# Kernel optimization log

Hardware: AMD Instinct MI355X
Metric: run time of the kernel (lower is better)

## Reference

```python
import jax, jax.numpy as jnp
import numpy as np

BN_EPS = 1e-3  # keras BatchNormalization default epsilon

def _prelu(x, a):
    return jnp.maximum(x, 0) + a * jnp.minimum(x, 0)

def _bn(x, g, b, m, v):
    # inference-mode batchnorm with moving statistics
    return (x - m) * jax.lax.rsqrt(v + BN_EPS) * g + b

def setup_inputs() -> dict:
    key = jax.random.key(0)
    ks = jax.random.split(key, 24)
    B, D, V, L = 4096, 768, 200000, 200000
    F = 3 * D  # 2304 = qid|pos|neg concat
    n = lambda i, shape, s=0.05: jax.random.normal(ks[i], shape, jnp.float32) * s
    return dict(
        qid_embeddings=jax.random.normal(ks[0], (B, D), jnp.float32),
        node_embeddings=n(1, (V, D), 0.1),
        leaf_embeddings=n(2, (L, D), 0.1),
        positives=jax.random.randint(ks[3], (B,), 0, V),
        negetives=jax.random.randint(ks[4], (B,), 0, V),
        p_isleafs=jax.random.randint(ks[5], (B,), 0, 2),
        n_isleafs=jax.random.randint(ks[6], (B,), 0, 2),
        W00=n(7, (F, 36)), b00=jnp.zeros((36,)), a00=jnp.full((36,), 0.25),
        W01=n(8, (36, 1)), b01=jnp.zeros((1,)),
        W1=n(9, (F, 128)), b1=jnp.zeros((128,)), a1=jnp.full((128,), 0.25),
        g1=jnp.ones((128,)), be1=n(10, (128,), 0.1), m1=n(11, (128,), 0.1),
        v1=jax.random.uniform(ks[12], (128,)) + 0.5,
        W2=n(13, (128, 64)), b2=jnp.zeros((64,)), a2=jnp.full((64,), 0.25),
        g2=jnp.ones((64,)), be2=n(14, (64,), 0.1), m2=n(15, (64,), 0.1),
        v2=jax.random.uniform(ks[16], (64,)) + 0.5,
        W3=n(17, (64, 24)), b3=jnp.zeros((24,)), a3=jnp.full((24,), 0.25),
        g3=jnp.ones((24,)), be3=n(18, (24,), 0.1), m3=n(19, (24,), 0.1),
        v3=jax.random.uniform(ks[20], (24,)) + 0.5,
        W4=n(21, (24, 2)), b4=jnp.zeros((2,)),
    )

def reference(qid_embeddings, node_embeddings, leaf_embeddings, positives, negetives,
              p_isleafs, n_isleafs, W00, b00, a00, W01, b01,
              W1, b1, a1, g1, be1, m1, v1,
              W2, b2, a2, g2, be2, m2, v2,
              W3, b3, a3, g3, be3, m3, v3, W4, b4):
    # per-sample conditional embedding gather (leaf table vs internal node table)
    pos = jnp.where((p_isleafs == 1)[:, None], leaf_embeddings[positives], node_embeddings[positives])  # [B,D]
    neg = jnp.where((n_isleafs == 1)[:, None], leaf_embeddings[negetives], node_embeddings[negetives])  # [B,D]
    q = qid_embeddings  # [B,D]
    # attention block: small Dense(36)->Dense(1) scalar weight per sample
    feat = jnp.concatenate([q, pos, neg], axis=1)  # [B,3D]
    h = _prelu(feat @ W00 + b00, a00)              # [B,36]
    w = h @ W01 + b01                              # [B,1]
    item = jnp.concatenate([w * pos, w * neg, q], axis=1)  # [B,3D]
    # MLP 2304 -> 128 -> 64 -> 24 -> 2 (layer10/20/30 unused in original call)
    x = _bn(_prelu(item @ W1 + b1, a1), g1, be1, m1, v1)
    x = _bn(_prelu(x @ W2 + b2, a2), g2, be2, m2, v2)
    x = _bn(_prelu(x @ W3 + b3, a3), g3, be3, m3, v3)
    return jax.nn.softmax(x @ W4 + b4, axis=-1)  # [B,2]
```

## Files before the change

kernel.cpp:

```cpp
#include <hip/hip_runtime.h>
#include <hip/hip_bf16.h>

typedef _Float16 half8 __attribute__((ext_vector_type(8)));
typedef _Float16 half4v __attribute__((ext_vector_type(4)));
typedef float f32x4 __attribute__((ext_vector_type(4)));

#define NCOLS 176
#define TILE_ELEMS (NCOLS*32)
#define TILE_U16 (TILE_ELEMS/8)
#define WTSTR 40
#define XSTR2 2312
#define BM 16

#define OFF_A36 0
#define OFF_TQ  2560
#define OFF_TPN 10752
#define OFF_WV  18944
#define OFF_X1  19008
#define OFF_W2  27456
#define OFF_X2  43840
#define OFF_W3  48192
#define OFF_X3  51264
#define OFF_SCR 53056
#define SM_BYTES 77632

struct Params {
  const float *qid, *node, *leaf;
  const int *pos_idx, *neg_idx, *p_leaf, *n_leaf;
  const float *b00, *a00, *W01, *b01;
  const float *b1, *a1, *g1, *be1, *m1, *v1;
  const float *W2, *b2, *a2, *g2, *be2, *m2, *v2;
  const float *W3, *b3, *a3, *g3, *be3, *m3, *v3;
  const float *W4, *b4;
  const _Float16 *Wp;
  float *out;
};

__global__ __launch_bounds__(256) void pack_weights(const float* __restrict__ W00,
                                                    const float* __restrict__ W1,
                                                    _Float16* __restrict__ Wp) {
  int g = blockIdx.x;
  int s = g / 24, t = g - s * 24;
  int k0 = t * 32;
  int w1row0 = (s == 0) ? 1536 : (s == 1 ? 0 : 768);
  __shared__ _Float16 T[NCOLS][WTSTR];
  int tid = threadIdx.x;
  for (int u = tid; u < 1024; u += 256) {
    int kk = u >> 5, c4 = u & 31;
    float4 f = *(const float4*)(W1 + (size_t)(w1row0 + k0 + kk) * 128 + c4 * 4);
    int c = 48 + c4 * 4;
    T[c + 0][kk] = (_Float16)f.x; T[c + 1][kk] = (_Float16)f.y;
    T[c + 2][kk] = (_Float16)f.z; T[c + 3][kk] = (_Float16)f.w;
  }
  for (int u = tid; u < 1152; u += 256) {
    int kk = u / 36, c = u - kk * 36;
    T[c][kk] = (_Float16)W00[(size_t)(s * 768 + k0 + kk) * 36 + c];
  }
  for (int u = tid; u < 384; u += 256) {
    int kk = u & 31, c = 36 + (u >> 5);
    T[c][kk] = (_Float16)0.f;
  }
  __syncthreads();
  uint4* dst = (uint4*)(Wp + (size_t)g * TILE_ELEMS);
  for (int u = tid; u < TILE_U16; u += 256) {
    int c = u >> 2, q = u & 3;
    dst[u] = *(const uint4*)&T[c][q * 8];
  }
}

__global__ __launch_bounds__(512) void fused_main(Params p) {
  __shared__ __align__(16) char sm[SM_BYTES];
  __shared__ const float* Xbase[3][BM];

  _Float16* X   = (_Float16*)sm;
  float*    A36 = (float*)(sm + OFF_A36);
  float*    Tq  = (float*)(sm + OFF_TQ);
  float*    Tpn = (float*)(sm + OFF_TPN);
  float*    wv  = (float*)(sm + OFF_WV);
  float*    x1  = (float*)(sm + OFF_X1);
  _Float16* W2h = (_Float16*)(sm + OFF_W2);
  float*    x2  = (float*)(sm + OFF_X2);
  _Float16* W3h = (_Float16*)(sm + OFF_W3);
  float*    x3  = (float*)(sm + OFF_X3);
  float*    scr = (float*)(sm + OFF_SCR);

  const int tid  = threadIdx.x;
  const int wid  = tid >> 6;
  const int lane = tid & 63;
  const int lm   = lane & 15;
  const int hk   = lane >> 4;
  const int nw   = wid & 3;
  const int kg   = wid >> 2;
  const int m0   = blockIdx.x * BM;
  const bool HAS2 = (nw < 3);

  const uint4* Wp4 = (const uint4*)p.Wp;
  const int woff = ((nw * 48 + lm) << 2) + hk;

  uint4 P[4][3];
  auto ldWp = [&](int j) {
    int s = j / 12;
    int g = s * 24 + kg + 2 * (j - s * 12);
    const uint4* b = Wp4 + (size_t)g * TILE_U16 + woff;
    P[j & 3][0] = b[0]; P[j & 3][1] = b[64];
    if (HAS2) P[j & 3][2] = b[128];
  };

  ldWp(0); ldWp(1); ldWp(2); ldWp(3);

  if (tid < 3 * BM) {
    int s = tid >> 4, i = tid & 15;
    const float* base;
    if (s == 0) base = p.qid + (size_t)(m0 + i) * 768;
    else if (s == 1) {
      int idx = p.pos_idx[m0 + i];
      base = ((p.p_leaf[m0 + i] == 1) ? p.leaf : p.node) + (size_t)idx * 768;
    } else {
      int idx = p.neg_idx[m0 + i];
      base = ((p.n_leaf[m0 + i] == 1) ? p.leaf : p.node) + (size_t)idx * 768;
    }
    Xbase[s][i] = base;
  }

  float4 sregA[6], sregB[6];
  auto stageLoad = [&](int s, float4* sr) {
#pragma unroll
    for (int jj = 0; jj < 6; ++jj) {
      int v = tid + jj * 512;
      int i = v / 192, c4 = v - i * 192;
      const float* b = (s == 0) ? (p.qid + (size_t)(m0 + i) * 768) : Xbase[s][i];
      sr[jj] = ((const float4*)b)[c4];
    }
  };
  auto stageWrite = [&](int s, const float4* sr) {
#pragma unroll
    for (int jj = 0; jj < 6; ++jj) {
      int v = tid + jj * 512;
      int i = v / 192, c4 = v - i * 192;
      float4 f = sr[jj];
      half4v h = { (_Float16)f.x, (_Float16)f.y, (_Float16)f.z, (_Float16)f.w };
      *(half4v*)(X + i * XSTR2 + s * 768 + c4 * 4) = h;
    }
  };

  stageLoad(0, sregA);
  __syncthreads();
  stageLoad(1, sregB);
  stageWrite(0, sregA);
  __syncthreads();

  f32x4 accA[3] = {{0.f,0.f,0.f,0.f},{0.f,0.f,0.f,0.f},{0.f,0.f,0.f,0.f}};
  f32x4 accB[3] = {{0.f,0.f,0.f,0.f},{0.f,0.f,0.f,0.f},{0.f,0.f,0.f,0.f}};
  half8 av[3];

  auto ldA = [&](int g) -> half8 {
    return *(const half8*)(X + lm * XSTR2 + g * 32 + hk * 8);
  };
  auto comp = [&](int g, int slot, half8 a) {
    half8 b0 = __builtin_bit_cast(half8, P[slot][0]);
    half8 b1 = __builtin_bit_cast(half8, P[slot][1]);
    half8 b2 = __builtin_bit_cast(half8, P[slot][2]);
    if ((nw == 0) || (g < 24)) {
      accA[0] = __builtin_amdgcn_mfma_f32_16x16x32_f16(a, b0, accA[0], 0, 0, 0);
      accA[1] = __builtin_amdgcn_mfma_f32_16x16x32_f16(a, b1, accA[1], 0, 0, 0);
      if (HAS2) accA[2] = __builtin_amdgcn_mfma_f32_16x16x32_f16(a, b2, accA[2], 0, 0, 0);
    } else {
      accB[0] = __builtin_amdgcn_mfma_f32_16x16x32_f16(a, b0, accB[0], 0, 0, 0);
      accB[1] = __builtin_amdgcn_mfma_f32_16x16x32_f16(a, b1, accB[1], 0, 0, 0);
      if (HAS2) accB[2] = __builtin_amdgcn_mfma_f32_16x16x32_f16(a, b2, accB[2], 0, 0, 0);
    }
  };

  float4 w2r[4];
#pragma unroll
  for (int s = 0; s < 3; ++s) {
    if (s == 1) {
      stageLoad(2, sregA);
      stageWrite(1, sregB);
      __syncthreads();
    }
    if (s == 2) {
#pragma unroll
      for (int jj = 0; jj < 4; ++jj) w2r[jj] = ((const float4*)p.W2)[tid + jj * 512];
      stageWrite(2, sregA);
      __syncthreads();
    }
    const int gb = s * 24 + kg;
    av[0] = ldA(gb); av[1] = ldA(gb + 2); av[2] = ldA(gb + 4);
#pragma unroll
    for (int tt = 0; tt < 12; ++tt) {
      int j = s * 12 + tt;
      comp(gb + 2 * tt, j & 3, av[tt % 3]);
      if (j + 4 < 36) ldWp(j + 4);
      if (tt + 3 < 12) av[tt % 3] = ldA(gb + 2 * (tt + 3));
    }
  }

  __syncthreads();
  if (kg == 1) {
#pragma unroll
    for (int n = 0; n < 3; ++n) {
      if (n < 2 || HAS2) {
#pragma unroll
        for (int r = 0; r < 4; ++r) {
          int base = ((nw * 3 + n) * 2) * 256 + (hk * 4 + r) * 16 + lm;
          scr[base]       = accA[n][r];
          scr[base + 256] = accB[n][r];
        }
      }
    }
  }
  __syncthreads();
  if (kg == 0) {
#pragma unroll
    for (int n = 0; n < 3; ++n) {
      if (n < 2 || HAS2) {
#pragma unroll
        for (int r = 0; r < 4; ++r) {
          int base = ((nw * 3 + n) * 2) * 256 + (hk * 4 + r) * 16 + lm;
          float va = accA[n][r] + scr[base];
          float vb = accB[n][r] + scr[base + 256];
          int row = hk * 4 + r;
          int col = nw * 48 + n * 16 + lm;
          if (nw == 0) { if (col < 36) A36[row * 40 + col] = va; }
          else { int rc = col - 48; Tq[row * 128 + rc] = va; Tpn[row * 128 + rc] = vb; }
        }
      }
    }
  }
  __syncthreads();

#pragma unroll
  for (int jj = 0; jj < 4; ++jj) {
    int u = tid + jj * 512;
    float4 f = w2r[jj];
    half4v h = { (_Float16)f.x, (_Float16)f.y, (_Float16)f.z, (_Float16)f.w };
    *(half4v*)(W2h + (u >> 4) * 64 + (u & 15) * 4) = h;
  }
  if (tid < BM) {
    float acc = p.b01[0];
    for (int c = 0; c < 36; ++c) {
      float h = A36[tid * 40 + c] + p.b00[c];
      h = (h > 0.f) ? h : p.a00[c] * h;
      acc += h * p.W01[c];
    }
    wv[tid] = acc;
  }
  __syncthreads();

#pragma unroll
  for (int j = 0; j < 4; ++j) {
    int u = tid + j * 512;
    int i = u >> 7, c = u & 127;
    float v = wv[i] * Tpn[i * 128 + c] + Tq[i * 128 + c] + p.b1[c];
    v = (v > 0.f) ? v : p.a1[c] * v;
    v = (v - p.m1[c]) * (1.f / sqrtf(p.v1[c] + 1e-3f)) * p.g1[c] + p.be1[c];
    x1[i * 132 + c] = v;
  }
  __syncthreads();

  if (tid < 256) {
    int i = tid & 15, cq = tid >> 4;
    const float* xr = x1 + i * 132;
    f32x4 acc0 = { p.b2[cq*4+0], p.b2[cq*4+1], p.b2[cq*4+2], p.b2[cq*4+3] };
    f32x4 acc1 = { 0.f, 0.f, 0.f, 0.f };
#pragma unroll 8
    for (int k = 0; k < 128; k += 2) {
      half4v w0 = *(const half4v*)(W2h + k * 64 + cq * 4);
      half4v w1 = *(const half4v*)(W2h + (k + 1) * 64 + cq * 4);
      acc0 += xr[k]     * __builtin_convertvector(w0, f32x4);
      acc1 += xr[k + 1] * __builtin_convertvector(w1, f32x4);
    }
    f32x4 acc = acc0 + acc1;
#pragma unroll
    for (int jj = 0; jj < 4; ++jj) {
      int c = cq * 4 + jj;
      float v = acc[jj];
      v = (v > 0.f) ? v : p.a2[c] * v;
      v = (v - p.m2[c]) * (1.f / sqrtf(p.v2[c] + 1e-3f)) * p.g2[c] + p.be2[c];
      x2[i * 68 + c] = v;
    }
  }
  for (int j = 0; j < 3; ++j) {
    int u = tid + j * 512;
    W3h[u] = (_Float16)p.W3[u];
  }
  __syncthreads();

  if (tid < 384) {
    int i = tid & 15, c = tid >> 4;
    float acc = p.b3[c];
#pragma unroll 8
    for (int k = 0; k < 64; ++k) acc += x2[i * 68 + k] * (float)W3h[k * 24 + c];
    acc = (acc > 0.f) ? acc : p.a3[c] * acc;
    acc = (acc - p.m3[c]) * (1.f / sqrtf(p.v3[c] + 1e-3f)) * p.g3[c] + p.be3[c];
    x3[i * 28 + c] = acc;
  }
  __syncthreads();

  if (tid < BM) {
    float l0 = p.b4[0], l1 = p.b4[1];
#pragma unroll
    for (int k = 0; k < 24; ++k) {
      float v = x3[tid * 28 + k];
      l0 += v * p.W4[k * 2 + 0];
      l1 += v * p.W4[k * 2 + 1];
    }
    float m = fmaxf(l0, l1);
    float e0 = __expf(l0 - m), e1 = __expf(l1 - m);
    float inv = 1.f / (e0 + e1);
    p.out[(size_t)(m0 + tid) * 2 + 0] = e0 * inv;
    p.out[(size_t)(m0 + tid) * 2 + 1] = e1 * inv;
  }
}

extern "C" void kernel_launch(void* const* d_in, const int* in_sizes, int n_in,
                              void* d_out, int out_size, void* d_ws, size_t ws_size,
                              hipStream_t stream) {
  const float* qid  = (const float*)d_in[0];
  const float* node = (const float*)d_in[1];
  const float* leaf = (const float*)d_in[2];
  const int* positives = (const int*)d_in[3];
  const int* negetives = (const int*)d_in[4];
  const int* p_isleafs = (const int*)d_in[5];
  const int* n_isleafs = (const int*)d_in[6];
  const float* W00 = (const float*)d_in[7];
  const float* b00 = (const float*)d_in[8];
  const float* a00 = (const float*)d_in[9];
  const float* W01 = (const float*)d_in[10];
  const float* b01 = (const float*)d_in[11];
  const float* W1  = (const float*)d_in[12];
  const float* b1  = (const float*)d_in[13];
  const float* a1  = (const float*)d_in[14];
  const float* g1  = (const float*)d_in[15];
  const float* be1 = (const float*)d_in[16];
  const float* m1  = (const float*)d_in[17];
  const float* v1  = (const float*)d_in[18];
  const float* W2  = (const float*)d_in[19];
  const float* b2  = (const float*)d_in[20];
  const float* a2  = (const float*)d_in[21];
  const float* g2  = (const float*)d_in[22];
  const float* be2 = (const float*)d_in[23];
  const float* m2  = (const float*)d_in[24];
  const float* v2  = (const float*)d_in[25];
  const float* W3  = (const float*)d_in[26];
  const float* b3  = (const float*)d_in[27];
  const float* a3  = (const float*)d_in[28];
  const float* g3  = (const float*)d_in[29];
  const float* be3 = (const float*)d_in[30];
  const float* m3  = (const float*)d_in[31];
  const float* v3  = (const float*)d_in[32];
  const float* W4  = (const float*)d_in[33];
  const float* b4  = (const float*)d_in[34];

  _Float16* Wp = (_Float16*)d_ws;

  pack_weights<<<72, 256, 0, stream>>>(W00, W1, Wp);

  Params p;
  p.qid = qid; p.node = node; p.leaf = leaf;
  p.pos_idx = positives; p.neg_idx = negetives; p.p_leaf = p_isleafs; p.n_leaf = n_isleafs;
  p.b00 = b00; p.a00 = a00; p.W01 = W01; p.b01 = b01;
  p.b1 = b1; p.a1 = a1; p.g1 = g1; p.be1 = be1; p.m1 = m1; p.v1 = v1;
  p.W2 = W2; p.b2 = b2; p.a2 = a2; p.g2 = g2; p.be2 = be2; p.m2 = m2; p.v2 = v2;
  p.W3 = W3; p.b3 = b3; p.a3 = a3; p.g3 = g3; p.be3 = be3; p.m3 = m3; p.v3 = v3;
  p.W4 = W4; p.b4 = b4;
  p.Wp = Wp;
  p.out = (float*)d_out;

  int B = in_sizes[3];
  fused_main<<<B / BM, 512, 0, stream>>>(p);
}
```

Before: 38.51 us.

## Issue all three gather stages upfront and use LDS-only barriers

Replaces __syncthreads with a custom barrier that waits only on LDS counters (lgkmcnt), so outstanding global loads are not drained at each barrier. All three row-stage gathers (q, pos, neg) are now issued before the first compute stage using a third register buffer, and the W2 prefetch moves earlier. This aims to hide global-memory latency behind the MFMA stages, at the cost of 24 extra VGPRs and a possible occupancy drop. The lgkmcnt-only barrier relies on vmem loads being consumed only after their own waitcnt.

```diff
diff --git a/kernel.cpp b/kernel.cpp
--- a/kernel.cpp
+++ b/kernel.cpp
@@ -11,6 +11,10 @@
 #define WTSTR 40
 #define XSTR2 2312
 #define BM 16
+
+#define BAR() do { asm volatile("s_waitcnt lgkmcnt(0)" ::: "memory"); \
+  __builtin_amdgcn_s_barrier(); \
+  __builtin_amdgcn_sched_barrier(0); } while (0)
 
 #define OFF_A36 0
 #define OFF_TQ  2560
@@ -122,7 +126,7 @@
     Xbase[s][i] = base;
   }
 
-  float4 sregA[6], sregB[6];
+  float4 sregA[6], sregB[6], sregC[6];
   auto stageLoad = [&](int s, float4* sr) {
 #pragma unroll
     for (int jj = 0; jj < 6; ++jj) {
@@ -143,11 +147,12 @@
     }
   };
 
+  BAR();
   stageLoad(0, sregA);
-  __syncthreads();
   stageLoad(1, sregB);
+  stageLoad(2, sregC);
   stageWrite(0, sregA);
-  __syncthreads();
+  BAR();
 
   f32x4 accA[3] = {{0.f,0.f,0.f,0.f},{0.f,0.f,0.f,0.f},{0.f,0.f,0.f,0.f}};
   f32x4 accB[3] = {{0.f,0.f,0.f,0.f},{0.f,0.f,0.f,0.f},{0.f,0.f,0.f,0.f}};
@@ -175,15 +180,14 @@
 #pragma unroll
   for (int s = 0; s < 3; ++s) {
     if (s == 1) {
-      stageLoad(2, sregA);
+#pragma unroll
+      for (int jj = 0; jj < 4; ++jj) w2r[jj] = ((const float4*)p.W2)[tid + jj * 512];
       stageWrite(1, sregB);
-      __syncthreads();
+      BAR();
     }
     if (s == 2) {
-#pragma unroll
-      for (int jj = 0; jj < 4; ++jj) w2r[jj] = ((const float4*)p.W2)[tid + jj * 512];
-      stageWrite(2, sregA);
-      __syncthreads();
+      stageWrite(2, sregC);
+      BAR();
     }
     const int gb = s * 24 + kg;
     av[0] = ldA(gb); av[1] = ldA(gb + 2); av[2] = ldA(gb + 4);
@@ -196,7 +200,7 @@
     }
   }
 
-  __syncthreads();
+  BAR();
   if (kg == 1) {
 #pragma unroll
     for (int n = 0; n < 3; ++n) {
@@ -210,7 +214,7 @@
       }
     }
   }
-  __syncthreads();
+  BAR();
   if (kg == 0) {
 #pragma unroll
     for (int n = 0; n < 3; ++n) {
@@ -228,7 +232,7 @@
       }
     }
   }
-  __syncthreads();
+  BAR();
 
 #pragma unroll
   for (int jj = 0; jj < 4; ++jj) {
@@ -246,7 +250,7 @@
     }
     wv[tid] = acc;
   }
-  __syncthreads();
+  BAR();
 
 #pragma unroll
   for (int j = 0; j < 4; ++j) {
@@ -257,7 +261,7 @@
     v = (v - p.m1[c]) * (1.f / sqrtf(p.v1[c] + 1e-3f)) * p.g1[c] + p.be1[c];
     x1[i * 132 + c] = v;
   }
-  __syncthreads();
+  BAR();
 
   if (tid < 256) {
     int i = tid & 15, cq = tid >> 4;
@@ -285,7 +289,7 @@
     int u = tid + j * 512;
     W3h[u] = (_Float16)p.W3[u];
   }
-  __syncthreads();
+  BAR();
 
   if (tid < 384) {
     int i = tid & 15, c = tid >> 4;
@@ -296,7 +300,7 @@
     acc = (acc - p.m3[c]) * (1.f / sqrtf(p.v3[c] + 1e-3f)) * p.g3[c] + p.be3[c];
     x3[i * 28 + c] = acc;
   }
-  __syncthreads();
+  BAR();
 
   if (tid < BM) {
     float l0 = p.b4[0], l1 = p.b4[1];
```

After: 41.18 us. +6.9%, slower.
